# Kernel tuning notes

Measured on AMD Instinct MI355X. Metric: run time of the kernel, lower is better.

## Reference

```python
import jax, jax.numpy as jnp
import numpy as np

N_HEADS = 8

def setup_inputs() -> dict:
    key = jax.random.key(0)
    ks = jax.random.split(key, 8)
    N, D, H = 20000, 16, 256
    scale = np.float32(0.02)
    return {
        "h": jax.random.normal(ks[0], (N, H), dtype=jnp.float32),
        "attention_mask": jnp.zeros((N,), dtype=jnp.float32),
        "neighbor_idx": jax.random.randint(ks[1], (N, D), 0, N, dtype=jnp.int32),
        "Wq": jax.random.normal(ks[2], (H, H), dtype=jnp.float32) * scale,
        "bq": jnp.zeros((H,), dtype=jnp.float32),
        "Wk": jax.random.normal(ks[3], (H, H), dtype=jnp.float32) * scale,
        "bk": jnp.zeros((H,), dtype=jnp.float32),
        "Wv": jax.random.normal(ks[4], (H, H), dtype=jnp.float32) * scale,
        "bv": jnp.zeros((H,), dtype=jnp.float32),
    }

def reference(h, attention_mask, neighbor_idx, Wq, bq, Wk, bk, Wv, bv):
    N, H = h.shape
    nh = N_HEADS
    dh = H // nh
    inv_sqrt_dh = np.float32(1.0 / np.sqrt(dh))
    # query from each node's own state: [N, nh, dh]
    q = (h @ Wq.T + bq).reshape(N, nh, dh)
    # gather neighbor mailbox: [N, D, H]
    nb = h[neighbor_idx]
    k = (nb @ Wk.T + bk).reshape(N, -1, nh, dh)  # [N, D, nh, dh]
    v = (nb @ Wv.T + bv).reshape(N, -1, nh, dh)
    # scores: [N, nh, D]
    scores = jnp.einsum('nhd,nkhd->nhk', q, k) * inv_sqrt_dh
    # additive mask gathered from source nodes, broadcast over heads
    scores = scores + attention_mask[neighbor_idx][:, None, :]
    probs = jax.nn.softmax(scores, axis=-1)
    # dropout prob = 0.0 (eval) -> identity
    ctx = jnp.einsum('nhk,nkhd->nhd', probs, v).reshape(N, H)
    return ctx
```

## Files before the change

### kernel.cpp

```cpp
#include <hip/hip_runtime.h>
#include <hip/hip_fp16.h>
#include <math.h>

#define HDIM 256
#define DNEIGH 16

typedef __attribute__((ext_vector_type(8))) short short8;
typedef __attribute__((ext_vector_type(4))) float f32x4;

static __device__ __forceinline__ unsigned short f2bf(float f) {
    unsigned int u = __float_as_uint(f);
    unsigned int r = (u + 0x7fffu + ((u >> 16) & 1u)) >> 16;
    return (unsigned short)r;
}
static __device__ __forceinline__ float bf_lo(unsigned int u) {
    return __uint_as_float(u << 16);
}
static __device__ __forceinline__ float bf_hi(unsigned int u) {
    return __uint_as_float(u & 0xffff0000u);
}

#if __has_builtin(__builtin_amdgcn_cvt_pk_fp8_f32)
static __device__ __forceinline__ unsigned char f2fp8(float v) {
    int pk = __builtin_amdgcn_cvt_pk_fp8_f32(v, v, 0, false);
    return (unsigned char)(pk & 0xff);
}
#else
static __device__ __forceinline__ unsigned char f2fp8(float v) {
    unsigned short h = __half_as_ushort(__float2half(v * (1.0f / 256.0f)));
    unsigned short mag = h & 0x7fffu;
    mag = (unsigned short)((mag + 0x40u) >> 7);
    if (mag > 0x7f) mag = 0x7f;
    return (unsigned char)(((h >> 8) & 0x80u) | mag);
}
#endif

#if __has_builtin(__builtin_amdgcn_cvt_f32_fp8)
#define FP8D(u, i) __builtin_amdgcn_cvt_f32_fp8((u), (i))
#else
static __device__ __forceinline__ float fp8_byte_dec(unsigned int b) {
    unsigned int hb = ((b & 0x80u) << 8) | ((b & 0x7fu) << 7);
    return __half2float(__ushort_as_half((unsigned short)hb)) * 256.0f;
}
#define FP8D(u, i) fp8_byte_dec(((u) >> ((i) * 8)) & 0xffu)
#endif

static __device__ __forceinline__ void async_copy16(const void* g, void* l) {
    __builtin_amdgcn_global_load_lds(
        (const __attribute__((address_space(1))) unsigned int*)g,
        (__attribute__((address_space(3))) unsigned int*)l, 16, 0, 0);
}

__global__ __launch_bounds__(256) void cvt_kernel(
    const float* __restrict__ h,
    const float* __restrict__ wq, const float* __restrict__ wk, const float* __restrict__ wv,
    unsigned short* __restrict__ hb,
    unsigned short* __restrict__ wqb, unsigned short* __restrict__ wkb, unsigned short* __restrict__ wvb,
    int nh4)
{
    const int stride = gridDim.x * blockDim.x;
    const int total = nh4 + 3 * 16384;
    for (int i = blockIdx.x * blockDim.x + threadIdx.x; i < total; i += stride) {
        const float4* src; unsigned short* dst; int off;
        if (i < nh4) { src = (const float4*)h; dst = hb; off = i; }
        else {
            int j = i - nh4; int s = j >> 14; off = j & 16383;
            src = (s == 0) ? (const float4*)wq : (s == 1) ? (const float4*)wk : (const float4*)wv;
            dst = (s == 0) ? wqb : (s == 1) ? wkb : wvb;
        }
        float4 v = src[off];
        ushort4 o;
        o.x = f2bf(v.x); o.y = f2bf(v.y); o.z = f2bf(v.z); o.w = f2bf(v.w);
        *(ushort4*)&dst[off * 4] = o;
    }
}

__global__ __launch_bounds__(256) void qkv_mfma_kernel(
    const unsigned short* __restrict__ hb,
    const unsigned short* __restrict__ Wqb,
    const unsigned short* __restrict__ Wkb,
    const unsigned short* __restrict__ Wvb,
    const float* __restrict__ bq, const float* __restrict__ bk, const float* __restrict__ bv,
    unsigned short* __restrict__ Qb, unsigned char* __restrict__ K8,
    unsigned short* __restrict__ Vb,
    int N)
{
    __shared__ unsigned short As[128 * 64];
    __shared__ unsigned short Bs[128 * 64];

    const int t = threadIdx.x;
    const int lane = t & 63;
    const int wid = t >> 6;
    const int wm = wid >> 1;
    const int wn = wid & 1;
    const int m0 = blockIdx.x * 128;
    const int o0 = blockIdx.y * 128;
    const int sel = o0 >> 8;
    const int wrow0 = o0 & 255;

    const unsigned short* __restrict__ W = (sel == 0) ? Wqb : (sel == 1) ? Wkb : Wvb;
    const float* __restrict__ bias = (sel == 0) ? bq : (sel == 1) ? bk : bv;

    const int srow = lane >> 3;
    const int cg = (lane & 7) ^ srow;

    f32x4 acc[4][4] = {};

    for (int k0 = 0; k0 < HDIM; k0 += 64) {
#pragma unroll
        for (int r = 0; r < 4; ++r) {
            int rowb = wid * 32 + r * 8;
            const unsigned short* gp = &hb[(size_t)(m0 + rowb + srow) * HDIM + k0 + cg * 8];
            async_copy16(gp, &As[rowb * 64]);
        }
#pragma unroll
        for (int r = 0; r < 4; ++r) {
            int rowb = wid * 32 + r * 8;
            const unsigned short* gp = &W[(size_t)(wrow0 + rowb + srow) * HDIM + k0 + cg * 8];
            async_copy16(gp, &Bs[rowb * 64]);
        }
        __syncthreads();

#pragma unroll
        for (int ks = 0; ks < 2; ++ks) {
            short8 af[4], bf[4];
#pragma unroll
            for (int i = 0; i < 4; ++i) {
                int m = wm * 64 + i * 16 + (lane & 15);
                int chunk = (ks * 4 + (lane >> 4)) ^ (m & 7);
                af[i] = *(const short8*)&As[m * 64 + chunk * 8];
            }
#pragma unroll
            for (int j = 0; j < 4; ++j) {
                int n = wn * 64 + j * 16 + (lane & 15);
                int chunk = (ks * 4 + (lane >> 4)) ^ (n & 7);
                bf[j] = *(const short8*)&Bs[n * 64 + chunk * 8];
            }
#pragma unroll
            for (int i = 0; i < 4; ++i)
#pragma unroll
                for (int j = 0; j < 4; ++j)
                    acc[i][j] = __builtin_amdgcn_mfma_f32_16x16x32_bf16(af[i], bf[j], acc[i][j], 0, 0, 0);
        }
        __syncthreads();
    }

#pragma unroll
    for (int i = 0; i < 4; ++i) {
        int mbase = m0 + wm * 64 + i * 16 + (lane >> 4) * 4;
#pragma unroll
        for (int j = 0; j < 4; ++j) {
            int col = wrow0 + wn * 64 + j * 16 + (lane & 15);
            float b = bias[col];
#pragma unroll
            for (int r = 0; r < 4; ++r) {
                int gr = mbase + r;
                if (gr < N) {
                    float v = acc[i][j][r] + b;
                    if (sel == 0)       Qb[(size_t)gr * HDIM + col] = f2bf(v);
                    else if (sel == 1)  K8[(size_t)gr * HDIM + col] = f2fp8(v);
                    else                Vb[(size_t)gr * HDIM + col] = f2bf(v);
                }
            }
        }
    }
}

__global__ __launch_bounds__(256) void attn4_kernel(
    const unsigned short* __restrict__ Qb,
    const unsigned char* __restrict__ K8,
    const unsigned short* __restrict__ Vb,
    const float* __restrict__ mask,
    const int* __restrict__ nidx,
    float* __restrict__ out,
    int N)
{
    const int w = threadIdx.x >> 6;
    const int lane = threadIdx.x & 63;
    const int n = blockIdx.x * 4 + w;
    if (n >= N) return;

    int idl = nidx[(size_t)n * DNEIGH + (lane & 15)];
    float mskl = mask[idl];

    unsigned int kreg[DNEIGH];
    uint2 vreg[DNEIGH];
#pragma unroll
    for (int d = 0; d < DNEIGH; ++d) {
        int id = __builtin_amdgcn_readlane(idl, d);
        kreg[d] = *(const unsigned int*)&K8[(size_t)id * HDIM + lane * 4];
        vreg[d] = *(const uint2*)&Vb[(size_t)id * HDIM + lane * 4];
    }

    uint2 qu = *(const uint2*)&Qb[(size_t)n * HDIM + lane * 4];
    const float q0 = bf_lo(qu.x), q1 = bf_hi(qu.x);
    const float q2 = bf_lo(qu.y), q3 = bf_hi(qu.y);

    float e[DNEIGH];
    float s = 0.f;
#pragma unroll
    for (int d = 0; d < DNEIGH; ++d) {
        float p = q0 * FP8D(kreg[d], 0) + q1 * FP8D(kreg[d], 1)
                + q2 * FP8D(kreg[d], 2) + q3 * FP8D(kreg[d], 3);
        p += __shfl_xor(p, 1);
        p += __shfl_xor(p, 2);
        p += __shfl_xor(p, 4);
        float mk = __int_as_float(__builtin_amdgcn_readlane(__float_as_int(mskl), d));
        e[d] = __expf(p * 0.17677669529663688f + mk);
        s += e[d];
    }
    float rs = 1.f / s;

    float4 acc = make_float4(0.f, 0.f, 0.f, 0.f);
#pragma unroll
    for (int d = 0; d < DNEIGH; ++d) {
        float wgt = e[d] * rs;
        acc.x += wgt * bf_lo(vreg[d].x);
        acc.y += wgt * bf_hi(vreg[d].x);
        acc.z += wgt * bf_lo(vreg[d].y);
        acc.w += wgt * bf_hi(vreg[d].y);
    }
    *(float4*)&out[(size_t)n * HDIM + lane * 4] = acc;
}

extern "C" void kernel_launch(void* const* d_in, const int* in_sizes, int n_in,
                              void* d_out, int out_size, void* d_ws, size_t ws_size,
                              hipStream_t stream)
{
    const float* h    = (const float*)d_in[0];
    const float* mask = (const float*)d_in[1];
    const int*   nidx = (const int*)d_in[2];
    const float* Wq   = (const float*)d_in[3];
    const float* bq   = (const float*)d_in[4];
    const float* Wk   = (const float*)d_in[5];
    const float* bk   = (const float*)d_in[6];
    const float* Wv   = (const float*)d_in[7];
    const float* bv   = (const float*)d_in[8];

    const int N = in_sizes[0] / HDIM;

    char* ws = (char*)d_ws;
    unsigned short* Qbp = (unsigned short*)ws; ws += (size_t)N * HDIM * 2;
    unsigned short* Vbp = (unsigned short*)ws; ws += (size_t)N * HDIM * 2;
    unsigned short* hbp = (unsigned short*)ws; ws += (size_t)N * HDIM * 2;
    unsigned char*  K8p = (unsigned char*)ws;  ws += (size_t)N * HDIM;
    unsigned short* Wqb = (unsigned short*)ws; ws += 65536 * 2;
    unsigned short* Wkb = (unsigned short*)ws; ws += 65536 * 2;
    unsigned short* Wvb = (unsigned short*)ws;

    const int nh4 = (N * HDIM) / 4;
    cvt_kernel<<<1280, 256, 0, stream>>>(h, Wq, Wk, Wv, hbp, Wqb, Wkb, Wvb, nh4);

    dim3 g1((N + 127) / 128, 6);
    qkv_mfma_kernel<<<g1, 256, 0, stream>>>(hbp, Wqb, Wkb, Wvb, bq, bk, bv, Qbp, K8p, Vbp, N);

    attn4_kernel<<<(N + 3) / 4, 256, 0, stream>>>(Qbp, K8p, Vbp, mask, nidx, (float*)d_out, N);
}
```

Baseline: 148.2 us.

## Swap MFMA operands for vectorized QKV epilogue stores; fold score scale into Q

The QKV GEMM swaps its A/B operands so each lane's four accumulator values lie along the channel dimension. This lets the epilogue issue packed 4-element stores and a float4 bias load instead of strided scalar stores. The 1/sqrt(dh) scale is folded into Q at write time, which removes a multiply per score in the attention kernel. The convert kernel now launches one thread per element instead of using a grid-stride loop, so it runs many more blocks.

```diff
diff --git a/kernel.cpp b/kernel.cpp
--- a/kernel.cpp
+++ b/kernel.cpp
@@ -58,21 +58,20 @@
     unsigned short* __restrict__ wqb, unsigned short* __restrict__ wkb, unsigned short* __restrict__ wvb,
     int nh4)
 {
-    const int stride = gridDim.x * blockDim.x;
+    int i = blockIdx.x * 256 + threadIdx.x;
     const int total = nh4 + 3 * 16384;
-    for (int i = blockIdx.x * blockDim.x + threadIdx.x; i < total; i += stride) {
-        const float4* src; unsigned short* dst; int off;
-        if (i < nh4) { src = (const float4*)h; dst = hb; off = i; }
-        else {
-            int j = i - nh4; int s = j >> 14; off = j & 16383;
-            src = (s == 0) ? (const float4*)wq : (s == 1) ? (const float4*)wk : (const float4*)wv;
-            dst = (s == 0) ? wqb : (s == 1) ? wkb : wvb;
-        }
-        float4 v = src[off];
-        ushort4 o;
-        o.x = f2bf(v.x); o.y = f2bf(v.y); o.z = f2bf(v.z); o.w = f2bf(v.w);
-        *(ushort4*)&dst[off * 4] = o;
-    }
+    if (i >= total) return;
+    const float4* src; unsigned short* dst; int off;
+    if (i < nh4) { src = (const float4*)h; dst = hb; off = i; }
+    else {
+        int j = i - nh4; int s = j >> 14; off = j & 16383;
+        src = (s == 0) ? (const float4*)wq : (s == 1) ? (const float4*)wk : (const float4*)wv;
+        dst = (s == 0) ? wqb : (s == 1) ? wkb : wvb;
+    }
+    float4 v = src[off];
+    ushort4 o;
+    o.x = f2bf(v.x); o.y = f2bf(v.y); o.z = f2bf(v.z); o.w = f2bf(v.w);
+    *(ushort4*)&dst[off * 4] = o;
 }
 
 __global__ __launch_bounds__(256) void qkv_mfma_kernel(
@@ -128,13 +127,13 @@
             for (int i = 0; i < 4; ++i) {
                 int m = wm * 64 + i * 16 + (lane & 15);
                 int chunk = (ks * 4 + (lane >> 4)) ^ (m & 7);
-                af[i] = *(const short8*)&As[m * 64 + chunk * 8];
+                af[i] = *(const short8*)&Bs[m * 64 + chunk * 8];
             }
 #pragma unroll
             for (int j = 0; j < 4; ++j) {
                 int n = wn * 64 + j * 16 + (lane & 15);
                 int chunk = (ks * 4 + (lane >> 4)) ^ (n & 7);
-                bf[j] = *(const short8*)&Bs[n * 64 + chunk * 8];
+                bf[j] = *(const short8*)&As[n * 64 + chunk * 8];
             }
 #pragma unroll
             for (int i = 0; i < 4; ++i)
@@ -145,21 +144,32 @@
         __syncthreads();
     }
 
+    const float qscale = 0.17677669529663688f;
 #pragma unroll
     for (int i = 0; i < 4; ++i) {
-        int mbase = m0 + wm * 64 + i * 16 + (lane >> 4) * 4;
+        int ch = wrow0 + wm * 64 + i * 16 + (lane >> 4) * 4;
+        float4 b4 = *(const float4*)&bias[ch];
 #pragma unroll
         for (int j = 0; j < 4; ++j) {
-            int col = wrow0 + wn * 64 + j * 16 + (lane & 15);
-            float b = bias[col];
-#pragma unroll
-            for (int r = 0; r < 4; ++r) {
-                int gr = mbase + r;
-                if (gr < N) {
-                    float v = acc[i][j][r] + b;
-                    if (sel == 0)       Qb[(size_t)gr * HDIM + col] = f2bf(v);
-                    else if (sel == 1)  K8[(size_t)gr * HDIM + col] = f2fp8(v);
-                    else                Vb[(size_t)gr * HDIM + col] = f2bf(v);
+            int node = m0 + wn * 64 + j * 16 + (lane & 15);
+            if (node < N) {
+                float v0 = acc[i][j][0] + b4.x;
+                float v1 = acc[i][j][1] + b4.y;
+                float v2 = acc[i][j][2] + b4.z;
+                float v3 = acc[i][j][3] + b4.w;
+                if (sel == 0) {
+                    ushort4 o;
+                    o.x = f2bf(v0 * qscale); o.y = f2bf(v1 * qscale);
+                    o.z = f2bf(v2 * qscale); o.w = f2bf(v3 * qscale);
+                    *(ushort4*)&Qb[(size_t)node * HDIM + ch] = o;
+                } else if (sel == 1) {
+                    uchar4 o;
+                    o.x = f2fp8(v0); o.y = f2fp8(v1); o.z = f2fp8(v2); o.w = f2fp8(v3);
+                    *(uchar4*)&K8[(size_t)node * HDIM + ch] = o;
+                } else {
+                    ushort4 o;
+                    o.x = f2bf(v0); o.y = f2bf(v1); o.z = f2bf(v2); o.w = f2bf(v3);
+                    *(ushort4*)&Vb[(size_t)node * HDIM + ch] = o;
                 }
             }
         }
@@ -206,7 +216,7 @@
         p += __shfl_xor(p, 2);
         p += __shfl_xor(p, 4);
         float mk = __int_as_float(__builtin_amdgcn_readlane(__float_as_int(mskl), d));
-        e[d] = __expf(p * 0.17677669529663688f + mk);
+        e[d] = __expf(p + mk);
         s += e[d];
     }
     float rs = 1.f / s;
@@ -249,7 +259,8 @@
     unsigned short* Wvb = (unsigned short*)ws;
 
     const int nh4 = (N * HDIM) / 4;
-    cvt_kernel<<<1280, 256, 0, stream>>>(h, Wq, Wk, Wv, hbp, Wqb, Wkb, Wvb, nh4);
+    const int total = nh4 + 3 * 16384;
+    cvt_kernel<<<(total + 255) / 256, 256, 0, stream>>>(h, Wq, Wk, Wv, hbp, Wqb, Wkb, Wvb, nh4);
 
     dim3 g1((N + 127) / 128, 6);
     qkv_mfma_kernel<<<g1, 256, 0, stream>>>(hbp, Wqb, Wkb, Wvb, bq, bk, bv, Qbp, K8p, Vbp, N);
```

New measurement: 142.8 us. 1.04x faster.
